# Performance work log

Hardware: AMD Instinct MI355X
Metric: run time of the kernel (lower is better)

## Reference

```python
import jax, jax.numpy as jnp
import numpy as np

B, C, D, H, W = 16, 8, 511, 16, 16
NHEADS = 16
DIM = C * H * W          # 2048 hidden size
SEQ = D + 1              # 512 tokens incl. cls
HEAD_DIM = DIM // NHEADS # 128


def setup_inputs() -> dict:
    key = jax.random.key(0)
    ks = jax.random.split(key, 8)
    s = 0.02  # weight init scale
    return {
        "x": jax.random.normal(ks[0], (B, C, D, H, W), jnp.float32),
        "pos_embedding": jax.random.normal(ks[1], (1, SEQ, DIM), jnp.float32),
        "cls": jax.random.normal(ks[2], (1, 1, DIM), jnp.float32),
        "qkv_w": jax.random.normal(ks[3], (DIM, 3 * DIM), jnp.float32) * s,
        "qkv_b": jnp.zeros((3 * DIM,), jnp.float32),
        "proj_w": jax.random.normal(ks[4], (DIM, DIM), jnp.float32) * s,
        "proj_b": jnp.zeros((DIM,), jnp.float32),
    }


def reference(x, pos_embedding, cls, qkv_w, qkv_b, proj_w, proj_b):
    b = x.shape[0]
    # rearrange 'b c d h w -> b d (c h w)'
    tok = jnp.transpose(x, (0, 2, 1, 3, 4)).reshape(b, D, DIM)
    tok = jnp.concatenate([jnp.broadcast_to(cls, (b, 1, DIM)), tok], axis=1)
    tok = tok + pos_embedding  # (b, SEQ, DIM)
    # qkv projection (dropout probs are 0 -> identity)
    qkv = tok @ qkv_w + qkv_b  # (b, SEQ, 3*DIM)
    qkv = qkv.reshape(b, SEQ, 3, NHEADS, HEAD_DIM).transpose(2, 0, 3, 1, 4)
    q, k, v = qkv[0], qkv[1], qkv[2]  # each (b, nH, SEQ, hd)
    scale = HEAD_DIM ** -0.5
    score = jax.nn.softmax(jnp.einsum('bhqd,bhkd->bhqk', q, k) * scale, axis=-1)
    out = jnp.einsum('bhqk,bhkd->bhqd', score, v)
    out = out.transpose(0, 2, 1, 3).reshape(b, SEQ, DIM)
    out = out @ proj_w + proj_b
    return out[:, 0]  # cls token, (b, DIM)
```

## Files before the change

kernel.cpp:

```cpp
#include <hip/hip_runtime.h>


#define BB   16
#define CC   8
#define DD   511
#define DIM  2048
#define SEQ  512
#define NH   16
#define HD   128
#define W3   6144
#define SCALE 0.08838834764831845f

#define QP_OFF  0
#define G_OFF   131072
#define AO_OFF  131088
#define SCP_OFF 163856
#define SCPSZ   131072
#define R_OFF   688144
#define RB_OFF  720912
#define U_OFF   753680

#define PSTR 520
#define CJ   32
#define TSTR 68

typedef __attribute__((ext_vector_type(8))) short short8;
typedef __attribute__((ext_vector_type(4))) float floatx4;

static __device__ inline short bf_hi(float f) {
  return (short)(__float_as_uint(f) >> 16);
}
static __device__ inline float bf_hif(float f) {
  return __uint_as_float(__float_as_uint(f) & 0xffff0000u);
}

__global__ __launch_bounds__(256) void k1_q(
    const float* __restrict__ pos, const float* __restrict__ cls,
    const float* __restrict__ qkv_w, const float* __restrict__ qkv_b,
    float* __restrict__ ws, float* __restrict__ out) {
  int n  = blockIdx.x * 256 + threadIdx.x;
  int dc = blockIdx.y;
  int tid = (blockIdx.x + blockIdx.y * 8) * 256 + threadIdx.x;
  if (tid < 32784) ws[G_OFF + tid] = 0.f;
  if (tid < BB * DIM) out[tid] = 0.f;
  int d0 = dc * 32;
  float acc = (dc == 0) ? qkv_b[n] : 0.f;
#pragma unroll 8
  for (int d = d0; d < d0 + 32; ++d) {
    float t0 = cls[d] + pos[d];
    acc += t0 * qkv_w[(size_t)d * W3 + n];
  }
  ws[QP_OFF + dc * DIM + n] = acc;
}

__global__ __launch_bounds__(128) void k2_r(
    const float* __restrict__ qkv_w, const float* __restrict__ pos,
    const float* __restrict__ cls, float* __restrict__ ws) {
  __shared__ float qs[HD];
  int h = blockIdx.y;
  int d = blockIdx.x * 128 + threadIdx.x;
  float qa = 0.f;
#pragma unroll 8
  for (int c = 0; c < 64; ++c)
    qa += ws[QP_OFF + c * DIM + h * HD + threadIdx.x];
  qs[threadIdx.x] = qa;
  __syncthreads();
  const float4* w4 = reinterpret_cast<const float4*>(
      qkv_w + (size_t)d * W3 + DIM + h * HD);
  float acc = 0.f;
#pragma unroll 8
  for (int e4 = 0; e4 < 32; ++e4) {
    float4 w = w4[e4];
    acc += qs[e4*4+0]*w.x + qs[e4*4+1]*w.y + qs[e4*4+2]*w.z + qs[e4*4+3]*w.w;
  }
  float r = acc * SCALE;
  int i = h * DIM + d;
  ws[R_OFF + i] = r;
  short* rb = (short*)(ws + RB_OFF);
  rb[i] = bf_hi(r);
  rb[NH * DIM + i] = bf_hi(r - bf_hif(r));
  float g = (cls[d] + pos[d]) * r;
  for (int m = 1; m < 64; m <<= 1) g += __shfl_xor(g, m, 64);
  if ((threadIdx.x & 63) == 0) atomicAdd(&ws[G_OFF + h], g);
}

__global__ __launch_bounds__(256) void k3_scores_mfma(
    const float* __restrict__ x, const float* __restrict__ pos,
    float* __restrict__ ws) {
  int jt2 = blockIdx.x, b = blockIdx.y, ks = blockIdx.z;
  int t = threadIdx.x;
  int w = t >> 6, l = t & 63;
  int jt = jt2 * 4 + w;
  int m16 = l & 15, kg = l >> 4;
  int jrow = 1 + jt * 16 + m16;
  int jc = jrow < SEQ ? jrow : (SEQ - 1);
  const size_t xrow = (size_t)b * CC * DD * 256 + (size_t)(jc - 1) * 256;
  const short* rh = (const short*)(ws + RB_OFF);
  const short* rl = rh + NH * DIM;
  floatx4 acc = {0.f, 0.f, 0.f, 0.f};
#pragma unroll 2
  for (int kk = ks * 16; kk < ks * 16 + 16; ++kk) {
    int d0 = kk * 32 + kg * 8;
    int c = d0 >> 8, doff = d0 & 255;
    const float4* xp = reinterpret_cast<const float4*>(
        x + xrow + (size_t)c * DD * 256 + doff);
    const float4* pp = reinterpret_cast<const float4*>(
        pos + (size_t)jc * DIM + d0);
    float4 xa = xp[0], xb = xp[1];
    float4 pa = pp[0], pb = pp[1];
    float f[8] = {xa.x + pa.x, xa.y + pa.y, xa.z + pa.z, xa.w + pa.w,
                  xb.x + pb.x, xb.y + pb.y, xb.z + pb.z, xb.w + pb.w};
    short8 ahi, alo;
#pragma unroll
    for (int i = 0; i < 8; ++i) {
      ahi[i] = bf_hi(f[i]);
      alo[i] = bf_hi(f[i] - bf_hif(f[i]));
    }
    short8 bhi = *reinterpret_cast<const short8*>(rh + m16 * DIM + d0);
    short8 blo = *reinterpret_cast<const short8*>(rl + m16 * DIM + d0);
    acc = __builtin_amdgcn_mfma_f32_16x16x32_bf16(ahi, bhi, acc, 0, 0, 0);
    acc = __builtin_amdgcn_mfma_f32_16x16x32_bf16(ahi, blo, acc, 0, 0, 0);
    acc = __builtin_amdgcn_mfma_f32_16x16x32_bf16(alo, bhi, acc, 0, 0, 0);
  }
  int h = m16;
#pragma unroll
  for (int reg = 0; reg < 4; ++reg) {
    int row = kg * 4 + reg;
    int j = 1 + jt * 16 + row;
    if (j < SEQ)
      ws[SCP_OFF + (size_t)ks * SCPSZ + (size_t)(b * NH + h) * SEQ + j] =
          acc[reg];
  }
}

__global__ __launch_bounds__(256) void k5_pv_mfma(
    const float* __restrict__ x, const float* __restrict__ pos,
    const float* __restrict__ cls, float* __restrict__ ws) {
  int dt = blockIdx.x, b = blockIdx.y, t = threadIdx.x;
  __shared__ __attribute__((aligned(16))) short phl[NH * PSTR];
  __shared__ __attribute__((aligned(16))) short pll[NH * PSTR];
  __shared__ short ths[2][CJ][TSTR];
  __shared__ short tls[2][CJ][TSTR];
  int w = t >> 6, l = t & 63;
  for (int rr = 0; rr < 4; ++rr) {
    int h = w * 4 + rr;
    const float* sc0 = ws + SCP_OFF + (size_t)(b * NH + h) * SEQ;
    float gam = ws[G_OFF + h];
    float s[8];
#pragma unroll
    for (int i = 0; i < 8; ++i) {
      int j = i * 64 + l;
      s[i] = sc0[j] + sc0[SCPSZ + j] + sc0[2 * SCPSZ + j] + sc0[3 * SCPSZ + j];
    }
    if (l == 0) s[0] = gam;
    float mx = s[0];
#pragma unroll
    for (int i = 1; i < 8; ++i) mx = fmaxf(mx, s[i]);
    for (int m = 1; m < 64; m <<= 1) mx = fmaxf(mx, __shfl_xor(mx, m, 64));
    float e[8], sum = 0.f;
#pragma unroll
    for (int i = 0; i < 8; ++i) { e[i] = __expf(s[i] - mx); sum += e[i]; }
    for (int m = 1; m < 64; m <<= 1) sum += __shfl_xor(sum, m, 64);
    float inv = 1.f / sum;
#pragma unroll
    for (int i = 0; i < 8; ++i) {
      float p = e[i] * inv;
      int j = i * 64 + l;
      phl[h * PSTR + j] = bf_hi(p);
      pll[h * PSTR + j] = bf_hi(p - bf_hif(p));
    }
  }
  const size_t xb = (size_t)b * CC * DD * 256;
  auto stage = [&](int kk, int buf) {
#pragma unroll
    for (int rep = 0; rep < 2; ++rep) {
      int idx = rep * 256 + t;
      int jj = idx >> 4, f4 = idx & 15;
      int j = kk * CJ + jj;
      int dbase = dt * 64 + f4 * 4;
      float4 pv = *reinterpret_cast<const float4*>(pos + (size_t)j * DIM + dbase);
      float4 xv;
      if (j == 0) {
        xv = *reinterpret_cast<const float4*>(cls + dbase);
      } else {
        int c = dbase >> 8, doff = dbase & 255;
        xv = *reinterpret_cast<const float4*>(
            x + xb + (size_t)c * DD * 256 + (size_t)(j - 1) * 256 + doff);
      }
      float f[4] = {xv.x + pv.x, xv.y + pv.y, xv.z + pv.z, xv.w + pv.w};
#pragma unroll
      for (int k = 0; k < 4; ++k) {
        ths[buf][jj][f4 * 4 + k] = bf_hi(f[k]);
        tls[buf][jj][f4 * 4 + k] = bf_hi(f[k] - bf_hif(f[k]));
      }
    }
  };
  stage(0, 0);
  int m16 = l & 15, kq = l >> 4;
  int wd = w * 16 + m16;
  int dcol = dt * 64 + wd;
  const short8* pph = reinterpret_cast<const short8*>(&phl[m16 * PSTR]);
  const short8* ppl = reinterpret_cast<const short8*>(&pll[m16 * PSTR]);
  floatx4 acc = {0.f, 0.f, 0.f, 0.f};
  for (int kk = 0; kk < 16; ++kk) {
    __syncthreads();
    if (kk < 15) stage(kk + 1, (kk + 1) & 1);
    int buf = kk & 1;
    short8 thi, tlo;
#pragma unroll
    for (int i = 0; i < 8; ++i) {
      thi[i] = ths[buf][kq * 8 + i][wd];
      tlo[i] = tls[buf][kq * 8 + i][wd];
    }
    short8 phi = pph[kk * 4 + kq];
    short8 plo = ppl[kk * 4 + kq];
    acc = __builtin_amdgcn_mfma_f32_16x16x32_bf16(phi, thi, acc, 0, 0, 0);
    acc = __builtin_amdgcn_mfma_f32_16x16x32_bf16(phi, tlo, acc, 0, 0, 0);
    acc = __builtin_amdgcn_mfma_f32_16x16x32_bf16(plo, thi, acc, 0, 0, 0);
  }
  float* ub = ws + U_OFF + (size_t)b * NH * DIM + dcol;
#pragma unroll
  for (int reg = 0; reg < 4; ++reg)
    ub[(size_t)(kq * 4 + reg) * DIM] = acc[reg];
}

__global__ __launch_bounds__(256) void k6_ao(
    const float* __restrict__ qkv_w, const float* __restrict__ qkv_b,
    float* __restrict__ ws) {
  int nt = blockIdx.x, dc = blockIdx.y, t = threadIdx.x;
  int m = nt * 256 + t;
  int h0 = nt * 2;
  int d0 = dc * 32;
  __shared__ float us[2][32][20];
  for (int i = t; i < 2 * 32 * BB; i += 256) {
    int dd = i & 31, b = (i >> 5) & 15, hh = i >> 9;
    us[hh][dd][b] = ws[U_OFF + (size_t)(b * NH + h0 + hh) * DIM + d0 + dd];
  }
  __syncthreads();
  int hl = t >> 7;
  float acc[BB];
#pragma unroll
  for (int b = 0; b < BB; ++b) acc[b] = 0.f;
  const float* wcol = qkv_w + (size_t)d0 * W3 + 2 * DIM + m;
#pragma unroll 4
  for (int dd = 0; dd < 32; ++dd) {
    float w = wcol[(size_t)dd * W3];
    const float4* u4 = reinterpret_cast<const float4*>(&us[hl][dd][0]);
    float4 u0 = u4[0], u1 = u4[1], u2 = u4[2], u3 = u4[3];
    acc[0]  += u0.x * w; acc[1]  += u0.y * w; acc[2]  += u0.z * w; acc[3]  += u0.w * w;
    acc[4]  += u1.x * w; acc[5]  += u1.y * w; acc[6]  += u1.z * w; acc[7]  += u1.w * w;
    acc[8]  += u2.x * w; acc[9]  += u2.y * w; acc[10] += u2.z * w; acc[11] += u2.w * w;
    acc[12] += u3.x * w; acc[13] += u3.y * w; acc[14] += u3.z * w; acc[15] += u3.w * w;
  }
  float bias = (dc == 0) ? qkv_b[2 * DIM + m] : 0.f;
#pragma unroll
  for (int b = 0; b < BB; ++b)
    atomicAdd(&ws[AO_OFF + b * DIM + m], acc[b] + bias);
}

__global__ __launch_bounds__(256) void k7_out(
    const float* __restrict__ proj_w, const float* __restrict__ proj_b,
    const float* __restrict__ ws, float* __restrict__ out) {
  int nt = blockIdx.x, mc = blockIdx.y, t = threadIdx.x;
  int n = nt * 256 + t;
  int m0 = mc * 32;
  __shared__ float as[32][20];
  for (int i = t; i < 32 * BB; i += 256) {
    int mm = i & 31, b = i >> 5;
    as[mm][b] = ws[AO_OFF + b * DIM + m0 + mm];
  }
  __syncthreads();
  float acc[BB];
#pragma unroll
  for (int b = 0; b < BB; ++b) acc[b] = 0.f;
  const float* wcol = proj_w + (size_t)m0 * DIM + n;
#pragma unroll 4
  for (int mm = 0; mm < 32; ++mm) {
    float w = wcol[(size_t)mm * DIM];
    const float4* a4 = reinterpret_cast<const float4*>(&as[mm][0]);
    float4 a0 = a4[0], a1 = a4[1], a2 = a4[2], a3 = a4[3];
    acc[0]  += a0.x * w; acc[1]  += a0.y * w; acc[2]  += a0.z * w; acc[3]  += a0.w * w;
    acc[4]  += a1.x * w; acc[5]  += a1.y * w; acc[6]  += a1.z * w; acc[7]  += a1.w * w;
    acc[8]  += a2.x * w; acc[9]  += a2.y * w; acc[10] += a2.z * w; acc[11] += a2.w * w;
    acc[12] += a3.x * w; acc[13] += a3.y * w; acc[14] += a3.z * w; acc[15] += a3.w * w;
  }
  float bias = (mc == 0) ? proj_b[n] : 0.f;
#pragma unroll
  for (int b = 0; b < BB; ++b)
    atomicAdd(&out[b * DIM + n], acc[b] + bias);
}

extern "C" void kernel_launch(void* const* d_in, const int* in_sizes, int n_in,
                              void* d_out, int out_size, void* d_ws, size_t ws_size,
                              hipStream_t stream) {
  const float* x      = (const float*)d_in[0];
  const float* pos    = (const float*)d_in[1];
  const float* cls    = (const float*)d_in[2];
  const float* qkv_w  = (const float*)d_in[3];
  const float* qkv_b  = (const float*)d_in[4];
  const float* proj_w = (const float*)d_in[5];
  const float* proj_b = (const float*)d_in[6];
  float* ws  = (float*)d_ws;
  float* out = (float*)d_out;

  k1_q          <<<dim3(8, 64),     256, 0, stream>>>(pos, cls, qkv_w, qkv_b, ws, out);
  k2_r          <<<dim3(16, 16),    128, 0, stream>>>(qkv_w, pos, cls, ws);
  k3_scores_mfma<<<dim3(8, 16, 4),  256, 0, stream>>>(x, pos, ws);
  k5_pv_mfma    <<<dim3(32, 16),    256, 0, stream>>>(x, pos, cls, ws);
  k6_ao         <<<dim3(8, 64),     256, 0, stream>>>(qkv_w, qkv_b, ws);
  k7_out        <<<dim3(8, 64),     256, 0, stream>>>(proj_w, proj_b, ws, out);
}
```

Before: 221.5 us.

## Precompute bf16 split tokens and transposed copy, split softmax into own kernel

Measured after the change: 259.0 us. 1.17x slower.

```diff
diff --git a/kernel.cpp b/kernel.cpp
--- a/kernel.cpp
+++ b/kernel.cpp
@@ -11,18 +11,18 @@
 #define W3   6144
 #define SCALE 0.08838834764831845f
 
-#define QP_OFF  0
-#define G_OFF   131072
-#define AO_OFF  131088
-#define SCP_OFF 163856
-#define SCPSZ   131072
-#define R_OFF   688144
-#define RB_OFF  720912
-#define U_OFF   753680
-
-#define PSTR 520
-#define CJ   32
-#define TSTR 68
+#define QP_OFF   0
+#define G_OFF    131072
+#define AO_OFF   131088
+#define SCP_OFF  163856
+#define SCPSZ    131072
+#define RB_OFF   688144
+#define PB_OFF   720912
+#define U_OFF    851984
+#define TOKH_OFF 1376272
+#define TOKL_OFF 9764880
+#define TTH_OFF  18153488
+#define TTL_OFF  26542096
 
 typedef __attribute__((ext_vector_type(8))) short short8;
 typedef __attribute__((ext_vector_type(4))) float floatx4;
@@ -34,23 +34,87 @@
   return __uint_as_float(__float_as_uint(f) & 0xffff0000u);
 }
 
-__global__ __launch_bounds__(256) void k1_q(
-    const float* __restrict__ pos, const float* __restrict__ cls,
-    const float* __restrict__ qkv_w, const float* __restrict__ qkv_b,
-    float* __restrict__ ws, float* __restrict__ out) {
-  int n  = blockIdx.x * 256 + threadIdx.x;
-  int dc = blockIdx.y;
-  int tid = (blockIdx.x + blockIdx.y * 8) * 256 + threadIdx.x;
-  if (tid < 32784) ws[G_OFF + tid] = 0.f;
-  if (tid < BB * DIM) out[tid] = 0.f;
-  int d0 = dc * 32;
-  float acc = (dc == 0) ? qkv_b[n] : 0.f;
+#define LSTR 72
+
+__global__ __launch_bounds__(256) void k0_tok(
+    const float* __restrict__ x, const float* __restrict__ pos,
+    const float* __restrict__ cls, const float* __restrict__ qkv_w,
+    const float* __restrict__ qkv_b, float* __restrict__ ws,
+    float* __restrict__ out) {
+  int blk = blockIdx.x, t = threadIdx.x;
+  if (blk < 4096) {
+    int gid = blk * 256 + t;
+    if (gid < 32784) ws[G_OFF + gid] = 0.f;
+    if (gid < BB * DIM) out[gid] = 0.f;
+    int dt = blk & 31, jt = (blk >> 5) & 7, b = blk >> 8;
+    __shared__ __attribute__((aligned(16))) short lh[64 * LSTR];
+    __shared__ __attribute__((aligned(16))) short ll[64 * LSTR];
+    short* th = (short*)(ws + TOKH_OFF);
+    short* tl = (short*)(ws + TOKL_OFF);
+    const size_t xb = (size_t)b * CC * DD * 256;
+#pragma unroll
+    for (int rep = 0; rep < 2; ++rep) {
+      int g = rep * 256 + t;
+      int j_loc = g >> 3, dg = g & 7;
+      int j = jt * 64 + j_loc;
+      int d = dt * 64 + dg * 8;
+      const float* pp = pos + (size_t)j * DIM + d;
+      float4 pa = *reinterpret_cast<const float4*>(pp);
+      float4 pb = *reinterpret_cast<const float4*>(pp + 4);
+      float4 xa, xb4;
+      if (j == 0) {
+        xa  = *reinterpret_cast<const float4*>(cls + d);
+        xb4 = *reinterpret_cast<const float4*>(cls + d + 4);
+      } else {
+        const float* xr = x + xb + (size_t)(d >> 8) * DD * 256 +
+                          (size_t)(j - 1) * 256 + (d & 255);
+        xa  = *reinterpret_cast<const float4*>(xr);
+        xb4 = *reinterpret_cast<const float4*>(xr + 4);
+      }
+      float f[8] = {xa.x + pa.x,  xa.y + pa.y,  xa.z + pa.z,  xa.w + pa.w,
+                    xb4.x + pb.x, xb4.y + pb.y, xb4.z + pb.z, xb4.w + pb.w};
+      short8 hi, lo;
+#pragma unroll
+      for (int i = 0; i < 8; ++i) {
+        hi[i] = bf_hi(f[i]);
+        lo[i] = bf_hi(f[i] - bf_hif(f[i]));
+      }
+      size_t o = (size_t)(b * SEQ + j) * DIM + d;
+      *reinterpret_cast<short8*>(th + o) = hi;
+      *reinterpret_cast<short8*>(tl + o) = lo;
+      *reinterpret_cast<short8*>(lh + j_loc * LSTR + dg * 8) = hi;
+      *reinterpret_cast<short8*>(ll + j_loc * LSTR + dg * 8) = lo;
+    }
+    __syncthreads();
+    short* tth = (short*)(ws + TTH_OFF);
+    short* ttl = (short*)(ws + TTL_OFF);
+#pragma unroll
+    for (int rep = 0; rep < 2; ++rep) {
+      int c = rep * 256 + t;
+      int jc = c >> 6, d_loc = c & 63;
+      short8 hv, lv;
+#pragma unroll
+      for (int i = 0; i < 8; ++i) {
+        hv[i] = lh[(jc * 8 + i) * LSTR + d_loc];
+        lv[i] = ll[(jc * 8 + i) * LSTR + d_loc];
+      }
+      size_t o = (size_t)(b * DIM + dt * 64 + d_loc) * SEQ + jt * 64 + jc * 8;
+      *reinterpret_cast<short8*>(tth + o) = hv;
+      *reinterpret_cast<short8*>(ttl + o) = lv;
+    }
+  } else {
+    int bb = blk - 4096;
+    int nt = bb & 7, dc = bb >> 3;
+    int n = nt * 256 + t;
+    int d0 = dc * 32;
+    float acc = (dc == 0) ? qkv_b[n] : 0.f;
 #pragma unroll 8
-  for (int d = d0; d < d0 + 32; ++d) {
-    float t0 = cls[d] + pos[d];
-    acc += t0 * qkv_w[(size_t)d * W3 + n];
-  }
-  ws[QP_OFF + dc * DIM + n] = acc;
+    for (int d = d0; d < d0 + 32; ++d) {
+      float t0 = cls[d] + pos[d];
+      acc += t0 * qkv_w[(size_t)d * W3 + n];
+    }
+    ws[QP_OFF + dc * DIM + n] = acc;
+  }
 }
 
 __global__ __launch_bounds__(128) void k2_r(
@@ -75,7 +139,6 @@
   }
   float r = acc * SCALE;
   int i = h * DIM + d;
-  ws[R_OFF + i] = r;
   short* rb = (short*)(ws + RB_OFF);
   rb[i] = bf_hi(r);
   rb[NH * DIM + i] = bf_hi(r - bf_hif(r));
@@ -84,136 +147,92 @@
   if ((threadIdx.x & 63) == 0) atomicAdd(&ws[G_OFF + h], g);
 }
 
-__global__ __launch_bounds__(256) void k3_scores_mfma(
-    const float* __restrict__ x, const float* __restrict__ pos,
-    float* __restrict__ ws) {
+__global__ __launch_bounds__(256) void k3_scores_mfma(float* __restrict__ ws) {
   int jt2 = blockIdx.x, b = blockIdx.y, ks = blockIdx.z;
-  int t = threadIdx.x;
-  int w = t >> 6, l = t & 63;
+  int t = threadIdx.x, w = t >> 6, l = t & 63;
   int jt = jt2 * 4 + w;
-  int m16 = l & 15, kg = l >> 4;
-  int jrow = 1 + jt * 16 + m16;
-  int jc = jrow < SEQ ? jrow : (SEQ - 1);
-  const size_t xrow = (size_t)b * CC * DD * 256 + (size_t)(jc - 1) * 256;
+  int m16 = l & 15, kq = l >> 4;
+  int j = jt * 16 + m16;
   const short* rh = (const short*)(ws + RB_OFF);
   const short* rl = rh + NH * DIM;
+  const short* th = (const short*)(ws + TOKH_OFF);
+  const short* tl = (const short*)(ws + TOKL_OFF);
+  const short* ra = rh + m16 * DIM;
+  const short* rb = rl + m16 * DIM;
+  const short* ta = th + (size_t)(b * SEQ + j) * DIM;
+  const short* tb = tl + (size_t)(b * SEQ + j) * DIM;
   floatx4 acc = {0.f, 0.f, 0.f, 0.f};
-#pragma unroll 2
+#pragma unroll 4
   for (int kk = ks * 16; kk < ks * 16 + 16; ++kk) {
-    int d0 = kk * 32 + kg * 8;
-    int c = d0 >> 8, doff = d0 & 255;
-    const float4* xp = reinterpret_cast<const float4*>(
-        x + xrow + (size_t)c * DD * 256 + doff);
-    const float4* pp = reinterpret_cast<const float4*>(
-        pos + (size_t)jc * DIM + d0);
-    float4 xa = xp[0], xb = xp[1];
-    float4 pa = pp[0], pb = pp[1];
-    float f[8] = {xa.x + pa.x, xa.y + pa.y, xa.z + pa.z, xa.w + pa.w,
-                  xb.x + pb.x, xb.y + pb.y, xb.z + pb.z, xb.w + pb.w};
-    short8 ahi, alo;
-#pragma unroll
-    for (int i = 0; i < 8; ++i) {
-      ahi[i] = bf_hi(f[i]);
-      alo[i] = bf_hi(f[i] - bf_hif(f[i]));
-    }
-    short8 bhi = *reinterpret_cast<const short8*>(rh + m16 * DIM + d0);
-    short8 blo = *reinterpret_cast<const short8*>(rl + m16 * DIM + d0);
+    int d0 = kk * 32 + kq * 8;
+    short8 ahi = *reinterpret_cast<const short8*>(ra + d0);
+    short8 alo = *reinterpret_cast<const short8*>(rb + d0);
+    short8 bhi = *reinterpret_cast<const short8*>(ta + d0);
+    short8 blo = *reinterpret_cast<const short8*>(tb + d0);
     acc = __builtin_amdgcn_mfma_f32_16x16x32_bf16(ahi, bhi, acc, 0, 0, 0);
+    acc = __builtin_amdgcn_mfma_f32_16x16x32_bf16(alo, bhi, acc, 0, 0, 0);
     acc = __builtin_amdgcn_mfma_f32_16x16x32_bf16(ahi, blo, acc, 0, 0, 0);
-    acc = __builtin_amdgcn_mfma_f32_16x16x32_bf16(alo, bhi, acc, 0, 0, 0);
-  }
-  int h = m16;
+  }
+  float* sc = ws + SCP_OFF + (size_t)ks * SCPSZ + (size_t)b * NH * SEQ;
 #pragma unroll
   for (int reg = 0; reg < 4; ++reg) {
-    int row = kg * 4 + reg;
-    int j = 1 + jt * 16 + row;
-    if (j < SEQ)
-      ws[SCP_OFF + (size_t)ks * SCPSZ + (size_t)(b * NH + h) * SEQ + j] =
-          acc[reg];
-  }
-}
-
-__global__ __launch_bounds__(256) void k5_pv_mfma(
-    const float* __restrict__ x, const float* __restrict__ pos,
-    const float* __restrict__ cls, float* __restrict__ ws) {
+    int h = kq * 4 + reg;
+    sc[(size_t)h * SEQ + j] = acc[reg];
+  }
+}
+
+__global__ __launch_bounds__(64) void k4_softmax(float* __restrict__ ws) {
+  int h = blockIdx.x, b = blockIdx.y, l = threadIdx.x;
+  const float* sc0 = ws + SCP_OFF + (size_t)(b * NH + h) * SEQ;
+  float gam = ws[G_OFF + h];
+  float s[8];
+#pragma unroll
+  for (int i = 0; i < 8; ++i) {
+    int j = i * 64 + l;
+    s[i] = sc0[j] + sc0[SCPSZ + j] + sc0[2 * SCPSZ + j] + sc0[3 * SCPSZ + j];
+  }
+  if (l == 0) s[0] = gam;
+  float mx = s[0];
+#pragma unroll
+  for (int i = 1; i < 8; ++i) mx = fmaxf(mx, s[i]);
+  for (int m = 1; m < 64; m <<= 1) mx = fmaxf(mx, __shfl_xor(mx, m, 64));
+  float e[8], sum = 0.f;
+#pragma unroll
+  for (int i = 0; i < 8; ++i) { e[i] = __expf(s[i] - mx); sum += e[i]; }
+  for (int m = 1; m < 64; m <<= 1) sum += __shfl_xor(sum, m, 64);
+  float inv = 1.f / sum;
+  short* ph = (short*)(ws + PB_OFF);
+  short* pl = ph + NH * SEQ * BB;
+#pragma unroll
+  for (int i = 0; i < 8; ++i) {
+    float p = e[i] * inv;
+    int j = i * 64 + l;
+    ph[(b * NH + h) * SEQ + j] = bf_hi(p);
+    pl[(b * NH + h) * SEQ + j] = bf_hi(p - bf_hif(p));
+  }
+}
+
+__global__ __launch_bounds__(256) void k5_pv_mfma(float* __restrict__ ws) {
   int dt = blockIdx.x, b = blockIdx.y, t = threadIdx.x;
-  __shared__ __attribute__((aligned(16))) short phl[NH * PSTR];
-  __shared__ __attribute__((aligned(16))) short pll[NH * PSTR];
-  __shared__ short ths[2][CJ][TSTR];
-  __shared__ short tls[2][CJ][TSTR];
   int w = t >> 6, l = t & 63;
-  for (int rr = 0; rr < 4; ++rr) {
-    int h = w * 4 + rr;
-    const float* sc0 = ws + SCP_OFF + (size_t)(b * NH + h) * SEQ;
-    float gam = ws[G_OFF + h];
-    float s[8];
-#pragma unroll
-    for (int i = 0; i < 8; ++i) {
-      int j = i * 64 + l;
-      s[i] = sc0[j] + sc0[SCPSZ + j] + sc0[2 * SCPSZ + j] + sc0[3 * SCPSZ + j];
-    }
-    if (l == 0) s[0] = gam;
-    float mx = s[0];
-#pragma unroll
-    for (int i = 1; i < 8; ++i) mx = fmaxf(mx, s[i]);
-    for (int m = 1; m < 64; m <<= 1) mx = fmaxf(mx, __shfl_xor(mx, m, 64));
-    float e[8], sum = 0.f;
-#pragma unroll
-    for (int i = 0; i < 8; ++i) { e[i] = __expf(s[i] - mx); sum += e[i]; }
-    for (int m = 1; m < 64; m <<= 1) sum += __shfl_xor(sum, m, 64);
-    float inv = 1.f / sum;
-#pragma unroll
-    for (int i = 0; i < 8; ++i) {
-      float p = e[i] * inv;
-      int j = i * 64 + l;
-      phl[h * PSTR + j] = bf_hi(p);
-      pll[h * PSTR + j] = bf_hi(p - bf_hif(p));
-    }
-  }
-  const size_t xb = (size_t)b * CC * DD * 256;
-  auto stage = [&](int kk, int buf) {
-#pragma unroll
-    for (int rep = 0; rep < 2; ++rep) {
-      int idx = rep * 256 + t;
-      int jj = idx >> 4, f4 = idx & 15;
-      int j = kk * CJ + jj;
-      int dbase = dt * 64 + f4 * 4;
-      float4 pv = *reinterpret_cast<const float4*>(pos + (size_t)j * DIM + dbase);
-      float4 xv;
-      if (j == 0) {
-        xv = *reinterpret_cast<const float4*>(cls + dbase);
-      } else {
-        int c = dbase >> 8, doff = dbase & 255;
-        xv = *reinterpret_cast<const float4*>(
-            x + xb + (size_t)c * DD * 256 + (size_t)(j - 1) * 256 + doff);
-      }
-      float f[4] = {xv.x + pv.x, xv.y + pv.y, xv.z + pv.z, xv.w + pv.w};
-#pragma unroll
-      for (int k = 0; k < 4; ++k) {
-        ths[buf][jj][f4 * 4 + k] = bf_hi(f[k]);
-        tls[buf][jj][f4 * 4 + k] = bf_hi(f[k] - bf_hif(f[k]));
-      }
-    }
-  };
-  stage(0, 0);
   int m16 = l & 15, kq = l >> 4;
-  int wd = w * 16 + m16;
-  int dcol = dt * 64 + wd;
-  const short8* pph = reinterpret_cast<const short8*>(&phl[m16 * PSTR]);
-  const short8* ppl = reinterpret_cast<const short8*>(&pll[m16 * PSTR]);
+  int dcol = dt * 64 + w * 16 + m16;
+  const short* ph = (const short*)(ws + PB_OFF);
+  const short* pl = ph + NH * SEQ * BB;
+  const short* tth = (const short*)(ws + TTH_OFF);
+  const short* ttl = (const short*)(ws + TTL_OFF);
+  const short* pa = ph + (size_t)(b * NH + m16) * SEQ;
+  const short* pb = pl + (size_t)(b * NH + m16) * SEQ;
+  const short* va = tth + (size_t)(b * DIM + dcol) * SEQ;
+  const short* vb = ttl + (size_t)(b * DIM + dcol) * SEQ;
   floatx4 acc = {0.f, 0.f, 0.f, 0.f};
+#pragma unroll 4
   for (int kk = 0; kk < 16; ++kk) {
-    __syncthreads();
-    if (kk < 15) stage(kk + 1, (kk + 1) & 1);
-    int buf = kk & 1;
-    short8 thi, tlo;
-#pragma unroll
-    for (int i = 0; i < 8; ++i) {
-      thi[i] = ths[buf][kq * 8 + i][wd];
-      tlo[i] = tls[buf][kq * 8 + i][wd];
-    }
-    short8 phi = pph[kk * 4 + kq];
-    short8 plo = ppl[kk * 4 + kq];
+    int j0 = kk * 32 + kq * 8;
+    short8 phi = *reinterpret_cast<const short8*>(pa + j0);
+    short8 plo = *reinterpret_cast<const short8*>(pb + j0);
+    short8 thi = *reinterpret_cast<const short8*>(va + j0);
+    short8 tlo = *reinterpret_cast<const short8*>(vb + j0);
     acc = __builtin_amdgcn_mfma_f32_16x16x32_bf16(phi, thi, acc, 0, 0, 0);
     acc = __builtin_amdgcn_mfma_f32_16x16x32_bf16(phi, tlo, acc, 0, 0, 0);
     acc = __builtin_amdgcn_mfma_f32_16x16x32_bf16(plo, thi, acc, 0, 0, 0);
@@ -303,10 +322,11 @@
   float* ws  = (float*)d_ws;
   float* out = (float*)d_out;
 
-  k1_q          <<<dim3(8, 64),     256, 0, stream>>>(pos, cls, qkv_w, qkv_b, ws, out);
+  k0_tok        <<<dim3(4608),      256, 0, stream>>>(x, pos, cls, qkv_w, qkv_b, ws, out);
   k2_r          <<<dim3(16, 16),    128, 0, stream>>>(qkv_w, pos, cls, ws);
-  k3_scores_mfma<<<dim3(8, 16, 4),  256, 0, stream>>>(x, pos, ws);
-  k5_pv_mfma    <<<dim3(32, 16),    256, 0, stream>>>(x, pos, cls, ws);
+  k3_scores_mfma<<<dim3(8, 16, 4),  256, 0, stream>>>(ws);
+  k4_softmax    <<<dim3(16, 16),     64, 0, stream>>>(ws);
+  k5_pv_mfma    <<<dim3(32, 16),    256, 0, stream>>>(ws);
   k6_ao         <<<dim3(8, 64),     256, 0, stream>>>(qkv_w, qkv_b, ws);
   k7_out        <<<dim3(8, 64),     256, 0, stream>>>(proj_w, proj_b, ws, out);
 }
```

## Split PV over sequence chunks in fp32 and replace atomics with partial buffers

Applied to the files above, without the earlier changes.

After: 259.5 us. 1.17x slower.

```diff
diff --git a/kernel.cpp b/kernel.cpp
--- a/kernel.cpp
+++ b/kernel.cpp
@@ -11,18 +11,13 @@
 #define W3   6144
 #define SCALE 0.08838834764831845f
 
-#define QP_OFF  0
-#define G_OFF   131072
-#define AO_OFF  131088
-#define SCP_OFF 163856
-#define SCPSZ   131072
-#define R_OFF   688144
-#define RB_OFF  720912
-#define U_OFF   753680
-
-#define PSTR 520
-#define CJ   32
-#define TSTR 68
+#define QP_OFF   0
+#define G_OFF    131072
+#define SCP_OFF  131088
+#define SCPSZ    131072
+#define RB_OFF   655376
+#define UP_OFF   688144
+#define AOP_OFF  4882448
 
 typedef __attribute__((ext_vector_type(8))) short short8;
 typedef __attribute__((ext_vector_type(4))) float floatx4;
@@ -41,7 +36,7 @@
   int n  = blockIdx.x * 256 + threadIdx.x;
   int dc = blockIdx.y;
   int tid = (blockIdx.x + blockIdx.y * 8) * 256 + threadIdx.x;
-  if (tid < 32784) ws[G_OFF + tid] = 0.f;
+  if (tid < 16) ws[G_OFF + tid] = 0.f;
   if (tid < BB * DIM) out[tid] = 0.f;
   int d0 = dc * 32;
   float acc = (dc == 0) ? qkv_b[n] : 0.f;
@@ -75,7 +70,6 @@
   }
   float r = acc * SCALE;
   int i = h * DIM + d;
-  ws[R_OFF + i] = r;
   short* rb = (short*)(ws + RB_OFF);
   rb[i] = bf_hi(r);
   rb[NH * DIM + i] = bf_hi(r - bf_hif(r));
@@ -133,14 +127,11 @@
   }
 }
 
-__global__ __launch_bounds__(256) void k5_pv_mfma(
+__global__ __launch_bounds__(256) void k5_pv(
     const float* __restrict__ x, const float* __restrict__ pos,
     const float* __restrict__ cls, float* __restrict__ ws) {
-  int dt = blockIdx.x, b = blockIdx.y, t = threadIdx.x;
-  __shared__ __attribute__((aligned(16))) short phl[NH * PSTR];
-  __shared__ __attribute__((aligned(16))) short pll[NH * PSTR];
-  __shared__ short ths[2][CJ][TSTR];
-  __shared__ short tls[2][CJ][TSTR];
+  int dt = blockIdx.x, b = blockIdx.y, js = blockIdx.z, t = threadIdx.x;
+  __shared__ __attribute__((aligned(16))) float pT[64][20];
   int w = t >> 6, l = t & 63;
   for (int rr = 0; rr < 4; ++rr) {
     int h = w * 4 + rr;
@@ -162,132 +153,114 @@
     for (int i = 0; i < 8; ++i) { e[i] = __expf(s[i] - mx); sum += e[i]; }
     for (int m = 1; m < 64; m <<= 1) sum += __shfl_xor(sum, m, 64);
     float inv = 1.f / sum;
-#pragma unroll
-    for (int i = 0; i < 8; ++i) {
-      float p = e[i] * inv;
-      int j = i * 64 + l;
-      phl[h * PSTR + j] = bf_hi(p);
-      pll[h * PSTR + j] = bf_hi(p - bf_hif(p));
+    pT[l][h] = e[js] * inv;
+  }
+  __syncthreads();
+  int d = dt * 1024 + t * 4;
+  int c = d >> 8, doff = d & 255;
+  const float* xcol = x + (size_t)b * CC * DD * 256 + (size_t)c * DD * 256 + doff;
+  floatx4 acc[16];
+#pragma unroll
+  for (int h = 0; h < 16; ++h) acc[h] = (floatx4){0.f, 0.f, 0.f, 0.f};
+#pragma unroll 4
+  for (int jl = 0; jl < 64; ++jl) {
+    int j = js * 64 + jl;
+    floatx4 pv = *reinterpret_cast<const floatx4*>(pos + (size_t)j * DIM + d);
+    floatx4 xv = (j == 0)
+        ? *reinterpret_cast<const floatx4*>(cls + d)
+        : *reinterpret_cast<const floatx4*>(xcol + (size_t)(j - 1) * 256);
+    floatx4 tok = xv + pv;
+#pragma unroll
+    for (int h4 = 0; h4 < 4; ++h4) {
+      floatx4 p4 = *reinterpret_cast<const floatx4*>(&pT[jl][h4 * 4]);
+      acc[h4 * 4 + 0] += p4.x * tok;
+      acc[h4 * 4 + 1] += p4.y * tok;
+      acc[h4 * 4 + 2] += p4.z * tok;
+      acc[h4 * 4 + 3] += p4.w * tok;
     }
   }
-  const size_t xb = (size_t)b * CC * DD * 256;
-  auto stage = [&](int kk, int buf) {
-#pragma unroll
-    for (int rep = 0; rep < 2; ++rep) {
-      int idx = rep * 256 + t;
-      int jj = idx >> 4, f4 = idx & 15;
-      int j = kk * CJ + jj;
-      int dbase = dt * 64 + f4 * 4;
-      float4 pv = *reinterpret_cast<const float4*>(pos + (size_t)j * DIM + dbase);
-      float4 xv;
-      if (j == 0) {
-        xv = *reinterpret_cast<const float4*>(cls + dbase);
-      } else {
-        int c = dbase >> 8, doff = dbase & 255;
-        xv = *reinterpret_cast<const float4*>(
-            x + xb + (size_t)c * DD * 256 + (size_t)(j - 1) * 256 + doff);
-      }
-      float f[4] = {xv.x + pv.x, xv.y + pv.y, xv.z + pv.z, xv.w + pv.w};
-#pragma unroll
-      for (int k = 0; k < 4; ++k) {
-        ths[buf][jj][f4 * 4 + k] = bf_hi(f[k]);
-        tls[buf][jj][f4 * 4 + k] = bf_hi(f[k] - bf_hif(f[k]));
-      }
-    }
-  };
-  stage(0, 0);
-  int m16 = l & 15, kq = l >> 4;
-  int wd = w * 16 + m16;
-  int dcol = dt * 64 + wd;
-  const short8* pph = reinterpret_cast<const short8*>(&phl[m16 * PSTR]);
-  const short8* ppl = reinterpret_cast<const short8*>(&pll[m16 * PSTR]);
-  floatx4 acc = {0.f, 0.f, 0.f, 0.f};
-  for (int kk = 0; kk < 16; ++kk) {
-    __syncthreads();
-    if (kk < 15) stage(kk + 1, (kk + 1) & 1);
-    int buf = kk & 1;
-    short8 thi, tlo;
-#pragma unroll
-    for (int i = 0; i < 8; ++i) {
-      thi[i] = ths[buf][kq * 8 + i][wd];
-      tlo[i] = tls[buf][kq * 8 + i][wd];
-    }
-    short8 phi = pph[kk * 4 + kq];
-    short8 plo = ppl[kk * 4 + kq];
-    acc = __builtin_amdgcn_mfma_f32_16x16x32_bf16(phi, thi, acc, 0, 0, 0);
-    acc = __builtin_amdgcn_mfma_f32_16x16x32_bf16(phi, tlo, acc, 0, 0, 0);
-    acc = __builtin_amdgcn_mfma_f32_16x16x32_bf16(plo, thi, acc, 0, 0, 0);
-  }
-  float* ub = ws + U_OFF + (size_t)b * NH * DIM + dcol;
-#pragma unroll
-  for (int reg = 0; reg < 4; ++reg)
-    ub[(size_t)(kq * 4 + reg) * DIM] = acc[reg];
+  float* ub = ws + UP_OFF + (size_t)(js * 16 + b) * 16 * 2048 + d;
+#pragma unroll
+  for (int h = 0; h < 16; ++h)
+    *reinterpret_cast<floatx4*>(ub + (size_t)h * 2048) = acc[h];
 }
 
 __global__ __launch_bounds__(256) void k6_ao(
     const float* __restrict__ qkv_w, const float* __restrict__ qkv_b,
     float* __restrict__ ws) {
-  int nt = blockIdx.x, dc = blockIdx.y, t = threadIdx.x;
+  int nt = blockIdx.x, ks = blockIdx.y, t = threadIdx.x;
   int m = nt * 256 + t;
   int h0 = nt * 2;
-  int d0 = dc * 32;
-  __shared__ float us[2][32][20];
-  for (int i = t; i < 2 * 32 * BB; i += 256) {
-    int dd = i & 31, b = (i >> 5) & 15, hh = i >> 9;
-    us[hh][dd][b] = ws[U_OFF + (size_t)(b * NH + h0 + hh) * DIM + d0 + dd];
+  __shared__ __attribute__((aligned(16))) float us[2][128][20];
+  for (int s = t; s < 4096; s += 256) {
+    int dd = s & 127, bb = (s >> 7) & 15, hh = s >> 11;
+    float a = 0.f;
+#pragma unroll
+    for (int js = 0; js < 8; ++js)
+      a += ws[UP_OFF + (size_t)(js * 16 + bb) * 16 * 2048 +
+              (size_t)(h0 + hh) * 2048 + ks * 128 + dd];
+    us[hh][dd][bb] = a;
   }
   __syncthreads();
   int hl = t >> 7;
   float acc[BB];
 #pragma unroll
-  for (int b = 0; b < BB; ++b) acc[b] = 0.f;
-  const float* wcol = qkv_w + (size_t)d0 * W3 + 2 * DIM + m;
+  for (int bb = 0; bb < BB; ++bb) acc[bb] = 0.f;
+  const float* wcol = qkv_w + (size_t)(ks * 128) * W3 + 2 * DIM + m;
 #pragma unroll 4
-  for (int dd = 0; dd < 32; ++dd) {
-    float w = wcol[(size_t)dd * W3];
-    const float4* u4 = reinterpret_cast<const float4*>(&us[hl][dd][0]);
-    float4 u0 = u4[0], u1 = u4[1], u2 = u4[2], u3 = u4[3];
-    acc[0]  += u0.x * w; acc[1]  += u0.y * w; acc[2]  += u0.z * w; acc[3]  += u0.w * w;
-    acc[4]  += u1.x * w; acc[5]  += u1.y * w; acc[6]  += u1.z * w; acc[7]  += u1.w * w;
-    acc[8]  += u2.x * w; acc[9]  += u2.y * w; acc[10] += u2.z * w; acc[11] += u2.w * w;
-    acc[12] += u3.x * w; acc[13] += u3.y * w; acc[14] += u3.z * w; acc[15] += u3.w * w;
-  }
-  float bias = (dc == 0) ? qkv_b[2 * DIM + m] : 0.f;
-#pragma unroll
-  for (int b = 0; b < BB; ++b)
-    atomicAdd(&ws[AO_OFF + b * DIM + m], acc[b] + bias);
+  for (int dd = 0; dd < 128; ++dd) {
+    float wv = wcol[(size_t)dd * W3];
+    floatx4 u0 = *reinterpret_cast<const floatx4*>(&us[hl][dd][0]);
+    floatx4 u1 = *reinterpret_cast<const floatx4*>(&us[hl][dd][4]);
+    floatx4 u2 = *reinterpret_cast<const floatx4*>(&us[hl][dd][8]);
+    floatx4 u3 = *reinterpret_cast<const floatx4*>(&us[hl][dd][12]);
+    acc[0]  += u0.x * wv; acc[1]  += u0.y * wv; acc[2]  += u0.z * wv; acc[3]  += u0.w * wv;
+    acc[4]  += u1.x * wv; acc[5]  += u1.y * wv; acc[6]  += u1.z * wv; acc[7]  += u1.w * wv;
+    acc[8]  += u2.x * wv; acc[9]  += u2.y * wv; acc[10] += u2.z * wv; acc[11] += u2.w * wv;
+    acc[12] += u3.x * wv; acc[13] += u3.y * wv; acc[14] += u3.z * wv; acc[15] += u3.w * wv;
+  }
+  float bias = (ks == 0) ? qkv_b[2 * DIM + m] : 0.f;
+#pragma unroll
+  for (int bb = 0; bb < BB; ++bb)
+    ws[AOP_OFF + (size_t)(ks * 16 + bb) * 2048 + m] = acc[bb] + bias;
 }
 
 __global__ __launch_bounds__(256) void k7_out(
     const float* __restrict__ proj_w, const float* __restrict__ proj_b,
     const float* __restrict__ ws, float* __restrict__ out) {
-  int nt = blockIdx.x, mc = blockIdx.y, t = threadIdx.x;
+  int nt = blockIdx.x, ms = blockIdx.y, t = threadIdx.x;
   int n = nt * 256 + t;
-  int m0 = mc * 32;
-  __shared__ float as[32][20];
-  for (int i = t; i < 32 * BB; i += 256) {
-    int mm = i & 31, b = i >> 5;
-    as[mm][b] = ws[AO_OFF + b * DIM + m0 + mm];
+  int m0 = ms * 128;
+  __shared__ __attribute__((aligned(16))) float as[128][20];
+  for (int s = t; s < 2048; s += 256) {
+    int mm = s & 127, bb = s >> 7;
+    float a = 0.f;
+#pragma unroll
+    for (int ks = 0; ks < 16; ++ks)
+      a += ws[AOP_OFF + (size_t)(ks * 16 + bb) * 2048 + m0 + mm];
+    as[mm][bb] = a;
   }
   __syncthreads();
   float acc[BB];
 #pragma unroll
-  for (int b = 0; b < BB; ++b) acc[b] = 0.f;
+  for (int bb = 0; bb < BB; ++bb) acc[bb] = 0.f;
   const float* wcol = proj_w + (size_t)m0 * DIM + n;
 #pragma unroll 4
-  for (int mm = 0; mm < 32; ++mm) {
-    float w = wcol[(size_t)mm * DIM];
-    const float4* a4 = reinterpret_cast<const float4*>(&as[mm][0]);
-    float4 a0 = a4[0], a1 = a4[1], a2 = a4[2], a3 = a4[3];
-    acc[0]  += a0.x * w; acc[1]  += a0.y * w; acc[2]  += a0.z * w; acc[3]  += a0.w * w;
-    acc[4]  += a1.x * w; acc[5]  += a1.y * w; acc[6]  += a1.z * w; acc[7]  += a1.w * w;
-    acc[8]  += a2.x * w; acc[9]  += a2.y * w; acc[10] += a2.z * w; acc[11] += a2.w * w;
-    acc[12] += a3.x * w; acc[13] += a3.y * w; acc[14] += a3.z * w; acc[15] += a3.w * w;
-  }
-  float bias = (mc == 0) ? proj_b[n] : 0.f;
-#pragma unroll
-  for (int b = 0; b < BB; ++b)
-    atomicAdd(&out[b * DIM + n], acc[b] + bias);
+  for (int mm = 0; mm < 128; ++mm) {
+    float wv = wcol[(size_t)mm * DIM];
+    floatx4 a0 = *reinterpret_cast<const floatx4*>(&as[mm][0]);
+    floatx4 a1 = *reinterpret_cast<const floatx4*>(&as[mm][4]);
+    floatx4 a2 = *reinterpret_cast<const floatx4*>(&as[mm][8]);
+    floatx4 a3 = *reinterpret_cast<const floatx4*>(&as[mm][12]);
+    acc[0]  += a0.x * wv; acc[1]  += a0.y * wv; acc[2]  += a0.z * wv; acc[3]  += a0.w * wv;
+    acc[4]  += a1.x * wv; acc[5]  += a1.y * wv; acc[6]  += a1.z * wv; acc[7]  += a1.w * wv;
+    acc[8]  += a2.x * wv; acc[9]  += a2.y * wv; acc[10] += a2.z * wv; acc[11] += a2.w * wv;
+    acc[12] += a3.x * wv; acc[13] += a3.y * wv; acc[14] += a3.z * wv; acc[15] += a3.w * wv;
+  }
+  float bias = (ms == 0) ? proj_b[n] : 0.f;
+#pragma unroll
+  for (int bb = 0; bb < BB; ++bb)
+    atomicAdd(&out[bb * DIM + n], acc[bb] + bias);
 }
 
 extern "C" void kernel_launch(void* const* d_in, const int* in_sizes, int n_in,
@@ -303,10 +276,10 @@
   float* ws  = (float*)d_ws;
   float* out = (float*)d_out;
 
-  k1_q          <<<dim3(8, 64),     256, 0, stream>>>(pos, cls, qkv_w, qkv_b, ws, out);
-  k2_r          <<<dim3(16, 16),    128, 0, stream>>>(qkv_w, pos, cls, ws);
-  k3_scores_mfma<<<dim3(8, 16, 4),  256, 0, stream>>>(x, pos, ws);
-  k5_pv_mfma    <<<dim3(32, 16),    256, 0, stream>>>(x, pos, cls, ws);
-  k6_ao         <<<dim3(8, 64),     256, 0, stream>>>(qkv_w, qkv_b, ws);
-  k7_out        <<<dim3(8, 64),     256, 0, stream>>>(proj_w, proj_b, ws, out);
-}
+  k1_q          <<<dim3(8, 64),    256, 0, stream>>>(pos, cls, qkv_w, qkv_b, ws, out);
+  k2_r          <<<dim3(16, 16),   128, 0, stream>>>(qkv_w, pos, cls, ws);
+  k3_scores_mfma<<<dim3(8, 16, 4), 256, 0, stream>>>(x, pos, ws);
+  k5_pv         <<<dim3(2, 16, 8), 256, 0, stream>>>(x, pos, cls, ws);
+  k6_ao         <<<dim3(8, 16),    256, 0, stream>>>(qkv_w, qkv_b, ws);
+  k7_out        <<<dim3(8, 16),    256, 0, stream>>>(proj_w, proj_b, ws, out);
+}
```

## Split score kernel over 16 d-chunks with LDS staging and separate softmax kernel

Applied to the files above, without the earlier changes.

Result: no change. 219.8 us (-0.8%).

```diff
diff --git a/kernel.cpp b/kernel.cpp
--- a/kernel.cpp
+++ b/kernel.cpp
@@ -11,14 +11,14 @@
 #define W3   6144
 #define SCALE 0.08838834764831845f
 
-#define QP_OFF  0
-#define G_OFF   131072
-#define AO_OFF  131088
-#define SCP_OFF 163856
-#define SCPSZ   131072
-#define R_OFF   688144
-#define RB_OFF  720912
-#define U_OFF   753680
+#define QP_OFF   0
+#define G_OFF    131072
+#define AO_OFF   131088
+#define SCP_OFF  163856
+#define SCPSZ    131072
+#define RB_OFF   2261008
+#define PB_OFF   2293776
+#define U_OFF    2424848
 
 #define PSTR 520
 #define CJ   32
@@ -75,7 +75,6 @@
   }
   float r = acc * SCALE;
   int i = h * DIM + d;
-  ws[R_OFF + i] = r;
   short* rb = (short*)(ws + RB_OFF);
   rb[i] = bf_hi(r);
   rb[NH * DIM + i] = bf_hi(r - bf_hif(r));
@@ -87,37 +86,44 @@
 __global__ __launch_bounds__(256) void k3_scores_mfma(
     const float* __restrict__ x, const float* __restrict__ pos,
     float* __restrict__ ws) {
-  int jt2 = blockIdx.x, b = blockIdx.y, ks = blockIdx.z;
+  int jt = blockIdx.x, b = blockIdx.y, dc = blockIdx.z;
   int t = threadIdx.x;
+  __shared__ __attribute__((aligned(16))) short ths[64][136];
+  __shared__ __attribute__((aligned(16))) short tls[64][136];
+  const size_t xb = (size_t)b * CC * DD * 256;
+#pragma unroll
+  for (int i = 0; i < 8; ++i) {
+    int idx = i * 256 + t;
+    int r = idx >> 5;
+    int c4 = idx & 31;
+    int jr = 1 + jt * 64 + r;
+    if (jr > 511) jr = 511;
+    int d = dc * 128 + c4 * 4;
+    int cc = d >> 8, doff = d & 255;
+    float4 xv = *reinterpret_cast<const float4*>(
+        x + xb + (size_t)cc * DD * 256 + (size_t)(jr - 1) * 256 + doff);
+    float4 pv = *reinterpret_cast<const float4*>(pos + (size_t)jr * DIM + d);
+    float f[4] = {xv.x + pv.x, xv.y + pv.y, xv.z + pv.z, xv.w + pv.w};
+#pragma unroll
+    for (int k = 0; k < 4; ++k) {
+      ths[r][c4 * 4 + k] = bf_hi(f[k]);
+      tls[r][c4 * 4 + k] = bf_hi(f[k] - bf_hif(f[k]));
+    }
+  }
+  __syncthreads();
   int w = t >> 6, l = t & 63;
-  int jt = jt2 * 4 + w;
   int m16 = l & 15, kg = l >> 4;
-  int jrow = 1 + jt * 16 + m16;
-  int jc = jrow < SEQ ? jrow : (SEQ - 1);
-  const size_t xrow = (size_t)b * CC * DD * 256 + (size_t)(jc - 1) * 256;
   const short* rh = (const short*)(ws + RB_OFF);
   const short* rl = rh + NH * DIM;
   floatx4 acc = {0.f, 0.f, 0.f, 0.f};
-#pragma unroll 2
-  for (int kk = ks * 16; kk < ks * 16 + 16; ++kk) {
-    int d0 = kk * 32 + kg * 8;
-    int c = d0 >> 8, doff = d0 & 255;
-    const float4* xp = reinterpret_cast<const float4*>(
-        x + xrow + (size_t)c * DD * 256 + doff);
-    const float4* pp = reinterpret_cast<const float4*>(
-        pos + (size_t)jc * DIM + d0);
-    float4 xa = xp[0], xb = xp[1];
-    float4 pa = pp[0], pb = pp[1];
-    float f[8] = {xa.x + pa.x, xa.y + pa.y, xa.z + pa.z, xa.w + pa.w,
-                  xb.x + pb.x, xb.y + pb.y, xb.z + pb.z, xb.w + pb.w};
-    short8 ahi, alo;
-#pragma unroll
-    for (int i = 0; i < 8; ++i) {
-      ahi[i] = bf_hi(f[i]);
-      alo[i] = bf_hi(f[i] - bf_hif(f[i]));
-    }
-    short8 bhi = *reinterpret_cast<const short8*>(rh + m16 * DIM + d0);
-    short8 blo = *reinterpret_cast<const short8*>(rl + m16 * DIM + d0);
+#pragma unroll
+  for (int kk = 0; kk < 4; ++kk) {
+    int dl = kk * 32 + kg * 8;
+    int gd = dc * 128 + dl;
+    short8 ahi = *reinterpret_cast<const short8*>(&ths[w * 16 + m16][dl]);
+    short8 alo = *reinterpret_cast<const short8*>(&tls[w * 16 + m16][dl]);
+    short8 bhi = *reinterpret_cast<const short8*>(rh + m16 * DIM + gd);
+    short8 blo = *reinterpret_cast<const short8*>(rl + m16 * DIM + gd);
     acc = __builtin_amdgcn_mfma_f32_16x16x32_bf16(ahi, bhi, acc, 0, 0, 0);
     acc = __builtin_amdgcn_mfma_f32_16x16x32_bf16(ahi, blo, acc, 0, 0, 0);
     acc = __builtin_amdgcn_mfma_f32_16x16x32_bf16(alo, bhi, acc, 0, 0, 0);
@@ -125,11 +131,44 @@
   int h = m16;
 #pragma unroll
   for (int reg = 0; reg < 4; ++reg) {
-    int row = kg * 4 + reg;
-    int j = 1 + jt * 16 + row;
+    int j = 1 + jt * 64 + w * 16 + kg * 4 + reg;
     if (j < SEQ)
-      ws[SCP_OFF + (size_t)ks * SCPSZ + (size_t)(b * NH + h) * SEQ + j] =
+      ws[SCP_OFF + (size_t)dc * SCPSZ + (size_t)(b * NH + h) * SEQ + j] =
           acc[reg];
+  }
+}
+
+__global__ __launch_bounds__(64) void k4_softmax(float* __restrict__ ws) {
+  int h = blockIdx.x, b = blockIdx.y, l = threadIdx.x;
+  const float* sc0 = ws + SCP_OFF + (size_t)(b * NH + h) * SEQ;
+  float gam = ws[G_OFF + h];
+  float s[8];
+#pragma unroll
+  for (int i = 0; i < 8; ++i) {
+    int j = i * 64 + l;
+    float a = 0.f;
+#pragma unroll
+    for (int p = 0; p < 16; ++p) a += sc0[(size_t)p * SCPSZ + j];
+    s[i] = a;
+  }
+  if (l == 0) s[0] = gam;
+  float mx = s[0];
+#pragma unroll
+  for (int i = 1; i < 8; ++i) mx = fmaxf(mx, s[i]);
+  for (int m = 1; m < 64; m <<= 1) mx = fmaxf(mx, __shfl_xor(mx, m, 64));
+  float e[8], sum = 0.f;
+#pragma unroll
+  for (int i = 0; i < 8; ++i) { e[i] = __expf(s[i] - mx); sum += e[i]; }
+  for (int m = 1; m < 64; m <<= 1) sum += __shfl_xor(sum, m, 64);
+  float inv = 1.f / sum;
+  short* ph = (short*)(ws + PB_OFF);
+  short* pl = ph + NH * SEQ * BB;
+#pragma unroll
+  for (int i = 0; i < 8; ++i) {
+    float p = e[i] * inv;
+    int j = i * 64 + l;
+    ph[(size_t)(b * NH + h) * SEQ + j] = bf_hi(p);
+    pl[(size_t)(b * NH + h) * SEQ + j] = bf_hi(p - bf_hif(p));
   }
 }
 
@@ -142,33 +181,14 @@
   __shared__ short ths[2][CJ][TSTR];
   __shared__ short tls[2][CJ][TSTR];
   int w = t >> 6, l = t & 63;
-  for (int rr = 0; rr < 4; ++rr) {
-    int h = w * 4 + rr;
-    const float* sc0 = ws + SCP_OFF + (size_t)(b * NH + h) * SEQ;
-    float gam = ws[G_OFF + h];
-    float s[8];
-#pragma unroll
-    for (int i = 0; i < 8; ++i) {
-      int j = i * 64 + l;
-      s[i] = sc0[j] + sc0[SCPSZ + j] + sc0[2 * SCPSZ + j] + sc0[3 * SCPSZ + j];
-    }
-    if (l == 0) s[0] = gam;
-    float mx = s[0];
-#pragma unroll
-    for (int i = 1; i < 8; ++i) mx = fmaxf(mx, s[i]);
-    for (int m = 1; m < 64; m <<= 1) mx = fmaxf(mx, __shfl_xor(mx, m, 64));
-    float e[8], sum = 0.f;
-#pragma unroll
-    for (int i = 0; i < 8; ++i) { e[i] = __expf(s[i] - mx); sum += e[i]; }
-    for (int m = 1; m < 64; m <<= 1) sum += __shfl_xor(sum, m, 64);
-    float inv = 1.f / sum;
-#pragma unroll
-    for (int i = 0; i < 8; ++i) {
-      float p = e[i] * inv;
-      int j = i * 64 + l;
-      phl[h * PSTR + j] = bf_hi(p);
-      pll[h * PSTR + j] = bf_hi(p - bf_hif(p));
-    }
+  const short* phg = (const short*)(ws + PB_OFF);
+  const short* plg = phg + NH * SEQ * BB;
+  for (int s = t; s < NH * SEQ / 2; s += 256) {
+    int h = s >> 8, j2 = (s & 255) * 2;
+    *reinterpret_cast<int*>(&phl[h * PSTR + j2]) =
+        *reinterpret_cast<const int*>(&phg[(size_t)(b * NH + h) * SEQ + j2]);
+    *reinterpret_cast<int*>(&pll[h * PSTR + j2]) =
+        *reinterpret_cast<const int*>(&plg[(size_t)(b * NH + h) * SEQ + j2]);
   }
   const size_t xb = (size_t)b * CC * DD * 256;
   auto stage = [&](int kk, int buf) {
@@ -305,7 +325,8 @@
 
   k1_q          <<<dim3(8, 64),     256, 0, stream>>>(pos, cls, qkv_w, qkv_b, ws, out);
   k2_r          <<<dim3(16, 16),    128, 0, stream>>>(qkv_w, pos, cls, ws);
-  k3_scores_mfma<<<dim3(8, 16, 4),  256, 0, stream>>>(x, pos, ws);
+  k3_scores_mfma<<<dim3(8, 16, 16), 256, 0, stream>>>(x, pos, ws);
+  k4_softmax    <<<dim3(16, 16),     64, 0, stream>>>(ws);
   k5_pv_mfma    <<<dim3(32, 16),    256, 0, stream>>>(x, pos, cls, ws);
   k6_ao         <<<dim3(8, 64),     256, 0, stream>>>(qkv_w, qkv_b, ws);
   k7_out        <<<dim3(8, 64),     256, 0, stream>>>(proj_w, proj_b, ws, out);
```
